# Optimization experiments

Hardware: AMD Instinct MI355X
Metric: run time of the kernel (lower is better)

Reference implementation:

```python
import jax, jax.numpy as jnp
import numpy as np

DN = ('NCHW', 'OIHW', 'NCHW')


def conv2d(x, w, b):
    y = jax.lax.conv_general_dilated(x, w, (1, 1), 'SAME', dimension_numbers=DN)
    return y + b[None, :, None, None]


def dyn_filter(x, Wa, ba, Wb, bb, Wc, bc):
    # KPN-style head: predict 81 per-pixel 9x9 filter taps, softmax-normalized.
    h = jax.nn.relu(conv2d(x, Wa, ba))
    h = jax.nn.relu(conv2d(h, Wb, bb))
    f = conv2d(h, Wc, bc)            # (N, 81, H, W)
    return jax.nn.softmax(f, axis=1)


def apply_dynamic_conv(x, f):
    # Equivalent to pad(4) + unfold(9x9) + mul + sum, without materializing
    # the (N,81,H,W)*... patch tensor: accumulate 81 shifted slices.
    N, C, H, W = x.shape  # C == 1
    xp = jnp.pad(x, ((0, 0), (0, 0), (4, 4), (4, 4)))
    out = jnp.zeros((N, 1, H, W), x.dtype)
    for dy in range(9):
        for dx in range(9):
            k = dy * 9 + dx  # matches unfold(2).unfold(3).permute(0,1,4,5,2,3) tap order
            out = out + xp[:, :, dy:dy + H, dx:dx + W] * f[:, k:k + 1]
    return out


def nearest_resize(x, oh, ow):
    _, _, ih, iw = x.shape
    ri = jnp.arange(oh) * ih // oh   # matches torch F.interpolate mode='nearest'
    rj = jnp.arange(ow) * iw // ow
    return x[:, :, ri][:, :, :, rj]


def setup_inputs() -> dict:
    key = jax.random.key(0)
    ks = jax.random.split(key, 8)
    s = 0.05
    return {
        'x': jax.random.normal(ks[0], (2, 1, 512, 512), jnp.float32),
        'g': jax.random.normal(ks[1], (2, 1, 512, 512), jnp.float32),
        'fWa': jax.random.normal(ks[2], (5, 64, 1, 3, 3), jnp.float32) * s,
        'fba': jnp.zeros((5, 64), jnp.float32),
        'fWb': jax.random.normal(ks[3], (5, 64, 64, 3, 3), jnp.float32) * s,
        'fbb': jnp.zeros((5, 64), jnp.float32),
        'fWc': jax.random.normal(ks[4], (5, 81, 64, 3, 3), jnp.float32) * s,
        'fbc': jnp.zeros((5, 81), jnp.float32),
        'W2a': jax.random.normal(ks[5], (64, 5, 3, 3), jnp.float32) * s,
        'b2a': jnp.zeros((64,), jnp.float32),
        'W2b': jax.random.normal(ks[6], (1, 64, 3, 3), jnp.float32) * s,
        'b2b': jnp.zeros((1,), jnp.float32),
    }


def reference(x, g, fWa, fba, fWb, fbb, fWc, fbc, W2a, b2a, W2b, b2b):
    N, C, h, w = x.shape
    scales = [
        x,
        nearest_resize(x, h // 2, w // 2),
        nearest_resize(x, h // 4, w // 4),
        nearest_resize(x, h // 8, w // 8),
        g,
    ]
    outs = []
    for i, s in enumerate(scales):
        f = dyn_filter(s, fWa[i], fba[i], fWb[i], fbb[i], fWc[i], fbc[i])
        y = apply_dynamic_conv(s, f)
        if y.shape[2] != h or y.shape[3] != w:
            y = nearest_resize(y, h, w)
        outs.append(y)
    cat = jnp.concatenate(outs, axis=1)  # (N, 5, h, w)
    hid = jax.nn.relu(conv2d(cat, W2a, b2a))
    return conv2d(hid, W2b, b2b)
```

## Files before the change

### kernel.cpp

```cpp
#include <hip/hip_runtime.h>
#include <math.h>

typedef _Float16 half8 __attribute__((ext_vector_type(8)));
typedef _Float16 half4v __attribute__((ext_vector_type(4)));
typedef float f32x4 __attribute__((ext_vector_type(4)));

#define LOG2E 1.44269504f

typedef __attribute__((address_space(1))) const unsigned int gas_u32;
typedef __attribute__((address_space(3))) unsigned int las_u32;

__device__ __forceinline__ void gll16(const void* gsrc, void* ldst) {
  __builtin_amdgcn_global_load_lds((gas_u32*)gsrc, (las_u32*)ldst, 16, 0, 0);
}
__device__ __forceinline__ void gll4(const void* gsrc, void* ldst) {
  __builtin_amdgcn_global_load_lds((gas_u32*)gsrc, (las_u32*)ldst, 4, 0, 0);
}

__device__ __forceinline__ void pack_generic(int rem, int NT, int COUT, float scale,
                                             const float* __restrict__ src,
                                             _Float16* __restrict__ dst) {
  int j = rem & 7, lane = (rem >> 3) & 63, rest = rem >> 9;
  int t = rest % NT, s = rest / NT;
  int oc = t * 16 + (lane & 15);
  int tap = s >> 1;
  int ic = (s & 1) * 32 + ((lane >> 4) & 3) * 8 + j;
  float v = (oc < COUT) ? src[((size_t)oc * 64 + ic) * 9 + tap] * scale : 0.f;
  dst[rem] = (_Float16)v;
}

__global__ void prep_all_kernel(const float* __restrict__ fWa, const float* __restrict__ fWb,
                                const float* __restrict__ fWc, const float* __restrict__ W2a,
                                const float* __restrict__ W2b, const float* __restrict__ x,
                                _Float16* __restrict__ Bp1, _Float16* __restrict__ BpA,
                                _Float16* __restrict__ BpB, _Float16* __restrict__ Bpb,
                                _Float16* __restrict__ Bpc,
                                _Float16* __restrict__ s1, _Float16* __restrict__ s2,
                                _Float16* __restrict__ s3) {
  int idx = blockIdx.x * blockDim.x + threadIdx.x;
  if (idx < 184320) {
    int sc = idx / 36864, rem = idx - sc * 36864;
    pack_generic(rem, 4, 64, 1.f, fWb + sc * 36864, Bpb + sc * 36864);
  } else if (idx < 460800) {
    int i2 = idx - 184320;
    int sc = i2 / 55296, rem = i2 - sc * 55296;
    pack_generic(rem, 6, 81, LOG2E, fWc + sc * 46656, Bpc + sc * 55296);
  } else if (idx < 471040) {
    int i2 = idx - 460800;
    int sc = i2 >> 11, rem = i2 & 2047;
    int j = rem & 7, lane = (rem >> 3) & 63, nt = rem >> 9;
    int oc = nt * 16 + (lane & 15);
    int k = ((lane >> 4) & 3) * 8 + j;
    float v = (k < 9) ? fWa[sc * 576 + oc * 9 + k] : 0.f;
    Bp1[sc * 2048 + rem] = (_Float16)v;
  } else if (idx < 475136) {
    int rem = idx - 471040;
    int j = rem & 7, lane = (rem >> 3) & 63;
    int nt = (rem >> 9) & 3, s = rem >> 11;
    int oc = nt * 16 + (lane & 15);
    int k = s * 32 + ((lane >> 4) & 3) * 8 + j;
    float v = 0.f;
    if (k < 45) { int ic = k / 9, tap = k - ic * 9; v = W2a[(oc * 5 + ic) * 9 + tap]; }
    BpA[rem] = (_Float16)v;
  } else if (idx < 484352) {
    pack_generic(idx - 475136, 1, 1, 1.f, W2b, BpB);
  } else if (idx < 615424) {
    int i2 = idx - 484352;
    int n = i2 >> 16, p = i2 & 65535, rr = p >> 8, cc = p & 255;
    s1[i2] = (_Float16)x[(size_t)n * 262144 + (size_t)(rr * 2) * 512 + cc * 2];
  } else if (idx < 648192) {
    int i2 = idx - 615424;
    int n = i2 >> 14, p = i2 & 16383, rr = p >> 7, cc = p & 127;
    s2[i2] = (_Float16)x[(size_t)n * 262144 + (size_t)(rr * 4) * 512 + cc * 4];
  } else if (idx < 656384) {
    int i2 = idx - 648192;
    int n = i2 >> 12, p = i2 & 4095, rr = p >> 6, cc = p & 63;
    s3[i2] = (_Float16)x[(size_t)n * 262144 + (size_t)(rr * 8) * 512 + cc * 8];
  }
}

__device__ __forceinline__ int xcd_swizzle(int bid) {
  return (bid & 7) * 596 + (bid >> 3);
}

__device__ __forceinline__ void map_block(int bid, int& sc, int& n, int& bx, int& by,
                                          int& Hs, int& RS, int& h2off) {
  if (bid < 2048) { sc = 0; Hs = 512; RS = 1; h2off = 0;
    int t = bid; n = t >> 10; t &= 1023; by = t >> 5; bx = t & 31; }
  else if (bid < 4096) { sc = 4; Hs = 512; RS = 1; h2off = 33554432;
    int t = bid - 2048; n = t >> 10; t &= 1023; by = t >> 5; bx = t & 31; }
  else if (bid < 4608) { sc = 1; Hs = 256; RS = 2; h2off = 67108864;
    int t = bid - 4096; n = t >> 8; t &= 255; by = t >> 4; bx = t & 15; }
  else if (bid < 4736) { sc = 2; Hs = 128; RS = 4; h2off = 75497472;
    int t = bid - 4608; n = t >> 6; t &= 63; by = t >> 3; bx = t & 7; }
  else { sc = 3; Hs = 64; RS = 8; h2off = 77594624;
    int t = bid - 4736; n = t >> 4; t &= 15; by = t >> 2; bx = t & 3; }
}

__device__ __forceinline__ const void* pick_src(int sc, const float* x, const float* g,
                                                const _Float16* s1, const _Float16* s2,
                                                const _Float16* s3, int& sStr, bool& f16s) {
  if (sc == 0) { sStr = 262144; f16s = false; return x; }
  if (sc == 1) { sStr = 65536; f16s = true; return s1; }
  if (sc == 2) { sStr = 16384; f16s = true; return s2; }
  if (sc == 3) { sStr = 4096; f16s = true; return s3; }
  sStr = 262144; f16s = false; return g;
}

__device__ __forceinline__ float src_load(const void* p, bool f16s, size_t off) {
  return f16s ? (float)((const _Float16*)p)[off] : ((const float*)p)[off];
}

template <int NT>
__device__ __forceinline__ void stageB_tap(const half8* __restrict__ Bp,
                                           _Float16* __restrict__ Bsd,
                                           int t, int buf, int tid) {
  const int lane = tid & 63, wv = tid >> 6;
  const char* s = (const char*)(Bp + (size_t)t * NT * 128) + wv * NT * 256 + lane * 4;
  char* d = (char*)Bsd + (size_t)buf * NT * 2048 + wv * NT * 256;
#pragma unroll
  for (int i = 0; i < NT; ++i) gll4(s + i * 256, d + i * 256);
}

template <int NT>
__device__ __forceinline__ void stageB01(const half8* __restrict__ Bp,
                                         _Float16* __restrict__ Bsd, int tid) {
  stageB_tap<NT>(Bp, Bsd, 0, 0, tid);
  stageB_tap<NT>(Bp, Bsd, 1, 1, tid);
}

template <int MT, int NT, bool SWAP>
__device__ __forceinline__ void tap_loop_counted(const _Float16* __restrict__ slab,
                                                 const half8* __restrict__ Bp,
                                                 _Float16* __restrict__ Bsd,
                                                 f32x4 (&acc)[MT][NT], int tid) {
  const int lane = tid & 63;
  const int wv = tid >> 6;
  const int quad = lane >> 4;
  const int ln15 = lane & 15;
  auto tap_body = [&](int t, int buf) {
    const int dy = t / 3, dx = t - dy * 3;
    const int C = dx + ln15;
    const int cx = C & 7;
    const _Float16* bb = Bsd + (size_t)buf * NT * 1024;
#pragma unroll
    for (int h = 0; h < 2; ++h) {
      half8 bf[NT];
#pragma unroll
      for (int nt = 0; nt < NT; ++nt)
        bf[nt] = *(const half8*)(bb + h * NT * 512 + (nt * 64 + lane) * 8);
      half8 af[MT];
#pragma unroll
      for (int mt = 0; mt < MT; ++mt) {
        const int px = (wv * MT + mt + dy) * 18 + C;
        af[mt] = *(const half8*)(slab + (size_t)px * 64 + ((h * 4 + quad) ^ cx) * 8);
      }
      __builtin_amdgcn_s_setprio(1);
#pragma unroll
      for (int mt = 0; mt < MT; ++mt)
#pragma unroll
        for (int nt = 0; nt < NT; ++nt)
          acc[mt][nt] = SWAP
            ? __builtin_amdgcn_mfma_f32_16x16x32_f16(bf[nt], af[mt], acc[mt][nt], 0, 0, 0)
            : __builtin_amdgcn_mfma_f32_16x16x32_f16(af[mt], bf[nt], acc[mt][nt], 0, 0, 0);
      __builtin_amdgcn_s_setprio(0);
    }
  };
#pragma unroll 1
  for (int t = 0; t < 8; ++t) {
    if (t >= 1) stageB_tap<NT>(Bp, Bsd, t + 1, (t + 1) & 1, tid);
    asm volatile("s_waitcnt vmcnt(%0)" :: "n"(NT) : "memory");
    __builtin_amdgcn_s_barrier();
    asm volatile("" ::: "memory");
    tap_body(t, t & 1);
    asm volatile("s_waitcnt lgkmcnt(0)" ::: "memory");
    __builtin_amdgcn_s_barrier();
    asm volatile("" ::: "memory");
  }
  asm volatile("s_waitcnt vmcnt(0)" ::: "memory");
  __builtin_amdgcn_s_barrier();
  asm volatile("" ::: "memory");
  tap_body(8, 0);
}

template <int MT, int NT, int COUT, int COUTP, bool RELU, typename OutT>
__device__ __forceinline__ void mfma_body(const _Float16* slab, const half8* __restrict__ Bp,
                                          _Float16* __restrict__ Bsd,
                                          const float* __restrict__ bias,
                                          OutT* __restrict__ out,
                                          int H, int W, int gr0, int gc0, int tid) {
  f32x4 acc[MT][NT];
  const f32x4 zz = {0.f, 0.f, 0.f, 0.f};
#pragma unroll
  for (int mt = 0; mt < MT; ++mt)
#pragma unroll
    for (int nt = 0; nt < NT; ++nt) acc[mt][nt] = zz;
  tap_loop_counted<MT, NT, false>(slab, Bp, Bsd, acc, tid);
  const int lane = tid & 63;
  const int wv = tid >> 6;
  const int quad = lane >> 4;
  const int ln15 = lane & 15;
  float bvv[NT];
#pragma unroll
  for (int nt = 0; nt < NT; ++nt) {
    const int oc = nt * 16 + ln15;
    bvv[nt] = (oc < COUT) ? bias[oc] : 0.f;
  }
#pragma unroll
  for (int mt = 0; mt < MT; ++mt) {
    const int gr = gr0 + wv * MT + mt;
#pragma unroll
    for (int reg = 0; reg < 4; ++reg) {
      const int gc = gc0 + quad * 4 + reg;
#pragma unroll
      for (int nt = 0; nt < NT; ++nt) {
        const int oc = nt * 16 + ln15;
        float v = acc[mt][nt][reg] + bvv[nt];
        if (RELU) v = fmaxf(v, 0.f);
        if (oc < COUTP) out[((size_t)gr * W + gc) * COUTP + oc] = (OutT)v;
      }
    }
  }
}

__global__ __launch_bounds__(512, 4)
void conv12_ms_kernel(const float* __restrict__ x, const float* __restrict__ g,
                      const _Float16* __restrict__ s1, const _Float16* __restrict__ s2,
                      const _Float16* __restrict__ s3,
                      const half8* __restrict__ Bp1b, const float* __restrict__ fba,
                      const half8* __restrict__ Bpbb, const float* __restrict__ fbb,
                      _Float16* __restrict__ h2) {
  __shared__ float xs[20 * 20];
  __shared__ __align__(16) _Float16 slab[18 * 18 * 64];
  __shared__ __align__(16) _Float16 BsS[2 * 4096];
  int sc, n, bx, by, Hs, RS, h2off;
  map_block(xcd_swizzle(blockIdx.x), sc, n, bx, by, Hs, RS, h2off);
  int sStr; bool f16s;
  const void* src = pick_src(sc, x, g, s1, s2, s3, sStr, f16s);
  _Float16* out = h2 + h2off + (size_t)n * Hs * Hs * 64;
  const half8* Bp1 = Bp1b + sc * 256;
  const half8* Bp = Bpbb + sc * 4608;
  const float* ba = fba + sc * 64;
  const float* bb = fbb + sc * 64;
  const int H = Hs, W = Hs;
  const int tid = threadIdx.x;
  const int gr0 = by * 16, gc0 = bx * 16;
  stageB01<4>(Bp, BsS, tid);
  for (int i = tid; i < 400; i += 512) {
    int R = i / 20, C = i % 20;
    int gr = gr0 - 2 + R, gc = gc0 - 2 + C;
    xs[i] = (gr >= 0 && gr < H && gc >= 0 && gc < W)
                ? src_load(src, f16s, (size_t)n * sStr + (size_t)gr * W + gc) : 0.f;
  }
  __syncthreads();
  const int lane = tid & 63;
  const int wv = tid >> 6;
  const int quad = lane >> 4;
  const int ln15 = lane & 15;
  half8 bf1[4];
  float b1v[4][4];
#pragma unroll
  for (int nt = 0; nt < 4; ++nt) {
    bf1[nt] = Bp1[nt * 64 + lane];
#pragma unroll
    for (int reg = 0; reg < 4; ++reg) b1v[nt][reg] = ba[nt * 16 + quad * 4 + reg];
  }
  int off1[8];
  bool v1[8];
#pragma unroll
  for (int j = 0; j < 8; ++j) {
    int k = quad * 8 + j;
    v1[j] = (k < 9);
    off1[j] = v1[j] ? ((k / 3) * 20 + (k % 3)) : 0;
  }
  const f32x4 zz = {0.f, 0.f, 0.f, 0.f};
#pragma unroll 1
  for (int mt = wv; mt < 21; mt += 8) {
    int p = mt * 16 + ln15;
    int pcl = (p < 323) ? p : 323;
    int Rg = pcl / 18, Cg = pcl - Rg * 18;
    int base = Rg * 20 + Cg;
    half8 af;
#pragma unroll
    for (int j = 0; j < 8; ++j)
      af[j] = v1[j] ? (_Float16)xs[base + off1[j]] : (_Float16)0.f;
    f32x4 a1[4] = {zz, zz, zz, zz};
#pragma unroll
    for (int nt = 0; nt < 4; ++nt)
      a1[nt] = __builtin_amdgcn_mfma_f32_16x16x32_f16(bf1[nt], af, a1[nt], 0, 0, 0);
    if (p < 324) {
      int R2 = p / 18, C2 = p - R2 * 18;
      int gr = gr0 - 1 + R2, gc = gc0 - 1 + C2;
      bool inb = (gr >= 0 && gr < H && gc >= 0 && gc < W);
      _Float16* sb = slab + p * 64 + (quad & 1) * 4;
      const int csw = C2 & 7;
#pragma unroll
      for (int nt = 0; nt < 4; ++nt) {
        half4v w;
#pragma unroll
        for (int reg = 0; reg < 4; ++reg) {
          float v = inb ? fmaxf(a1[nt][reg] + b1v[nt][reg], 0.f) : 0.f;
          w[reg] = (_Float16)v;
        }
        const int chunk = nt * 2 + (quad >> 1);
        *(half4v*)(sb + ((chunk ^ csw) * 8)) = w;
      }
    }
  }
  __syncthreads();
  mfma_body<2, 4, 64, 64, true, _Float16>(slab, Bp, BsS, bb, out, H, W, gr0, gc0, tid);
}

__global__ __launch_bounds__(512, 2)
void conv3sd_ms_kernel(const _Float16* __restrict__ h2, const half8* __restrict__ Bpcb,
                       const float* __restrict__ fbc,
                       const float* __restrict__ x, const float* __restrict__ g,
                       const _Float16* __restrict__ s1, const _Float16* __restrict__ s2,
                       const _Float16* __restrict__ s3, float* __restrict__ cat) {
  __shared__ __align__(16) _Float16 slab[384 * 64];
  __shared__ __align__(16) _Float16 Bsd[2 * 6144];
  __shared__ float xs[24 * 24];
  int sc, n, bx, by, Hs, RS, h2off;
  map_block(xcd_swizzle(blockIdx.x), sc, n, bx, by, Hs, RS, h2off);
  int sStr; bool f16s;
  const void* src = pick_src(sc, x, g, s1, s2, s3, sStr, f16s);
  const _Float16* in = h2 + h2off + (size_t)n * Hs * Hs * 64;
  const half8* Bp = Bpcb + sc * 6912;
  const float* bias = fbc + sc * 81;
  float* catp = cat + (size_t)(sc * 2 + n) * 262144;
  const int H = Hs, W = Hs;
  const int tid = threadIdx.x;
  const int gr0 = by * 16, gc0 = bx * 16;
  const int lane = tid & 63;
  const int wv = tid >> 6;
  const int quad = lane >> 4;
  const int ln15 = lane & 15;

  for (int i = tid; i < 576; i += 512) {
    int R = i / 24, C = i % 24;
    int gr = gr0 - 4 + R, gc = gc0 - 4 + C;
    xs[i] = (gr >= 0 && gr < H && gc >= 0 && gc < W)
                ? src_load(src, f16s, (size_t)n * sStr + (size_t)gr * W + gc) : 0.f;
  }

  const bool interior = (gr0 > 0) && (gc0 > 0) && (gr0 + 17 <= H) && (gc0 + 17 <= W);
  if (interior) {
    const int pxb0 = wv * 48;
#pragma unroll
    for (int k = 0; k < 6; ++k) {
      const int pxb = pxb0 + k * 8;
      int px = pxb + (lane >> 3);
      int pcl = (px < 324) ? px : 323;
      int R = pcl / 18, C = pcl - R * 18;
      int l = (lane & 7) ^ (C & 7);
      gll16((const char*)(in + ((size_t)(gr0 - 1 + R) * W + (gc0 - 1 + C)) * 64 + l * 8),
            (char*)slab + (size_t)pxb * 128);
    }
  } else {
    for (int i = tid; i < 2592; i += 512) {
      int px = i >> 3, pslot = i & 7;
      int R = px / 18, C = px - R * 18;
      int gr = gr0 - 1 + R, gc = gc0 - 1 + C;
      int l = pslot ^ (C & 7);
      half8 v = {0, 0, 0, 0, 0, 0, 0, 0};
      if (gr >= 0 && gr < H && gc >= 0 && gc < W)
        v = *(const half8*)(in + ((size_t)gr * W + gc) * 64 + l * 8);
      *(half8*)(slab + (size_t)px * 64 + pslot * 8) = v;
    }
  }

  stageB01<6>(Bp, Bsd, tid);
  asm volatile("s_waitcnt lgkmcnt(0)" ::: "memory");

  f32x4 acc[2][6];
  const f32x4 zz = {0.f, 0.f, 0.f, 0.f};
#pragma unroll
  for (int mt = 0; mt < 2; ++mt)
#pragma unroll
    for (int nt = 0; nt < 6; ++nt) acc[mt][nt] = zz;
  tap_loop_counted<2, 6, true>(slab, Bp, Bsd, acc, tid);

  float bvv[6][4];
  int dyx[6][4];
  bool vv[6][4];
#pragma unroll
  for (int nt = 0; nt < 6; ++nt)
#pragma unroll
    for (int reg = 0; reg < 4; ++reg) {
      int ch = nt * 16 + quad * 4 + reg;
      bool ok = (ch < 81);
      vv[nt][reg] = ok;
      bvv[nt][reg] = ok ? bias[ch] * LOG2E : 0.f;
      int dy = ch / 9, dx = ch - dy * 9;
      dyx[nt][reg] = ok ? dy * 24 + dx : 0;
    }
  const int lrs = (RS == 2) ? 1 : ((RS == 4) ? 2 : 3);
#pragma unroll
  for (int mt = 0; mt < 2; ++mt) {
    const float* xb = xs + (wv * 2 + mt) * 24 + ln15;
    float sum = 0.f, y = 0.f;
#pragma unroll
    for (int nt = 0; nt < 6; ++nt)
#pragma unroll
      for (int reg = 0; reg < 4; ++reg) {
        if (vv[nt][reg]) {
          float e = exp2f(acc[mt][nt][reg] + bvv[nt][reg]);
          sum += e;
          y = fmaf(e, xb[dyx[nt][reg]], y);
        }
      }
    sum += __shfl_xor(sum, 16, 64);
    sum += __shfl_xor(sum, 32, 64);
    y += __shfl_xor(y, 16, 64);
    y += __shfl_xor(y, 32, 64);
    const float o = y / sum;
    const int gr = gr0 + wv * 2 + mt, gc = gc0 + ln15;
    if (RS == 1) {
      if (quad == 0) catp[(size_t)gr * 512 + gc] = o;
    } else {
      for (int t = quad; t < RS * RS; t += 4) {
        int a = t >> lrs, b = t & (RS - 1);
        catp[((size_t)(gr * RS + a)) * 512 + (gc * RS + b)] = o;
      }
    }
  }
}

__global__ __launch_bounds__(512, 4)
void tail_fused_kernel(const float* __restrict__ cat,
                       const half8* __restrict__ BpA, const float* __restrict__ b2a,
                       const half8* __restrict__ BpB, const float* __restrict__ b2b,
                       float* __restrict__ out) {
  __shared__ float cs[20 * 20 * 5];
  __shared__ __align__(16) _Float16 hid[18 * 18 * 64];
  __shared__ __align__(16) _Float16 BsS[2 * 1024];
  const int n = blockIdx.z;
  float* op = out + (size_t)n * (512 * 512);
  const int tid = threadIdx.x;
  const int gr0 = blockIdx.y * 16, gc0 = blockIdx.x * 16;
  stageB01<1>(BpB, BsS, tid);
  for (int i = tid; i < 2000; i += 512) {
    int ic = i / 400, px = i - ic * 400;
    int R = px / 20, C = px - R * 20;
    int gr = gr0 - 2 + R, gc = gc0 - 2 + C;
    cs[px * 5 + ic] = (gr >= 0 && gr < 512 && gc >= 0 && gc < 512)
                ? cat[(size_t)(ic * 2 + n) * 262144 + (size_t)gr * 512 + gc] : 0.f;
  }
  __syncthreads();
  const int lane = tid & 63;
  const int wv = tid >> 6;
  const int quad = lane >> 4;
  const int ln15 = lane & 15;
  int goff[2][8];
  bool gok[2][8];
#pragma unroll
  for (int s = 0; s < 2; ++s)
#pragma unroll
    for (int j = 0; j < 8; ++j) {
      int k = s * 32 + quad * 8 + j;
      bool ok = (k < 45);
      int ic = k / 9;
      int tap = k - ic * 9;
      int dy = tap / 3, dx = tap - dy * 3;
      goff[s][j] = ok ? ((dy * 20 + dx) * 5 + ic) : 0;
      gok[s][j] = ok;
    }
  half8 bfA[2][4];
  float bAv[4][4];
#pragma unroll
  for (int s = 0; s < 2; ++s)
#pragma unroll
    for (int nt = 0; nt < 4; ++nt) bfA[s][nt] = BpA[(s * 4 + nt) * 64 + lane];
#pragma unroll
  for (int nt = 0; nt < 4; ++nt)
#pragma unroll
    for (int reg = 0; reg < 4; ++reg) bAv[nt][reg] = b2a[nt * 16 + quad * 4 + reg];
  const f32x4 zz = {0.f, 0.f, 0.f, 0.f};
#pragma unroll 1
  for (int mt = wv; mt < 21; mt += 8) {
    int p = mt * 16 + ln15;
    int pcl = (p < 323) ? p : 323;
    int base = (pcl / 18) * 100 + (pcl % 18) * 5;
    f32x4 acc1[4] = {zz, zz, zz, zz};
#pragma unroll
    for (int s = 0; s < 2; ++s) {
      half8 af;
#pragma unroll
      for (int j = 0; j < 8; ++j) {
        float a = gok[s][j] ? cs[base + goff[s][j]] : 0.f;
        af[j] = (_Float16)a;
      }
#pragma unroll
      for (int nt = 0; nt < 4; ++nt)
        acc1[nt] = __builtin_amdgcn_mfma_f32_16x16x32_f16(bfA[s][nt], af, acc1[nt], 0, 0, 0);
    }
    if (p < 324) {
      int R2 = p / 18, C2 = p - R2 * 18;
      int gr = gr0 - 1 + R2, gc = gc0 - 1 + C2;
      bool inb = (gr >= 0 && gr < 512 && gc >= 0 && gc < 512);
      _Float16* sb = hid + p * 64 + (quad & 1) * 4;
      const int csw = C2 & 7;
#pragma unroll
      for (int nt = 0; nt < 4; ++nt) {
        half4v w;
#pragma unroll
        for (int reg = 0; reg < 4; ++reg) {
          float v = inb ? fmaxf(acc1[nt][reg] + bAv[nt][reg], 0.f) : 0.f;
          w[reg] = (_Float16)v;
        }
        const int chunk = nt * 2 + (quad >> 1);
        *(half4v*)(sb + ((chunk ^ csw) * 8)) = w;
      }
    }
  }
  __syncthreads();
  mfma_body<2, 1, 1, 1, false, float>(hid, BpB, BsS, b2b, op, 512, 512, gr0, gc0, tid);
}

extern "C" void kernel_launch(void* const* d_in, const int* in_sizes, int n_in,
                              void* d_out, int out_size, void* d_ws, size_t ws_size,
                              hipStream_t stream) {
  (void)in_sizes; (void)n_in; (void)out_size; (void)ws_size;
  const float* x   = (const float*)d_in[0];
  const float* g   = (const float*)d_in[1];
  const float* fWa = (const float*)d_in[2];
  const float* fba = (const float*)d_in[3];
  const float* fWb = (const float*)d_in[4];
  const float* fbb = (const float*)d_in[5];
  const float* fWc = (const float*)d_in[6];
  const float* fbc = (const float*)d_in[7];
  const float* W2a = (const float*)d_in[8];
  const float* b2a = (const float*)d_in[9];
  const float* W2b = (const float*)d_in[10];
  const float* b2b = (const float*)d_in[11];
  float* out = (float*)d_out;
  float* ws = (float*)d_ws;

  float* Bp1F = ws;
  float* BpAF = Bp1F + 5120;
  float* BpBF = BpAF + 2048;
  float* BpbF = BpBF + 4608;
  float* BpcF = BpbF + 92160;
  float* s1F  = BpcF + 138240;
  float* s2F  = s1F + 65536;
  float* s3F  = s2F + 16384;
  float* cat  = s3F + 4096;
  float* h2F  = cat + 2621440;
  _Float16* s1 = (_Float16*)s1F;
  _Float16* s2 = (_Float16*)s2F;
  _Float16* s3 = (_Float16*)s3F;
  _Float16* h2 = (_Float16*)h2F;
  const half8* Bp1 = (const half8*)Bp1F;
  const half8* BpA = (const half8*)BpAF;
  const half8* BpB = (const half8*)BpBF;
  const half8* Bpb = (const half8*)BpbF;
  const half8* Bpc = (const half8*)BpcF;

  prep_all_kernel<<<2564, 256, 0, stream>>>(fWa, fWb, fWc, W2a, W2b, x,
                                            (_Float16*)Bp1F, (_Float16*)BpAF,
                                            (_Float16*)BpBF, (_Float16*)BpbF,
                                            (_Float16*)BpcF, s1, s2, s3);
  conv12_ms_kernel<<<4768, 512, 0, stream>>>(x, g, s1, s2, s3, Bp1, fba, Bpb, fbb, h2);
  conv3sd_ms_kernel<<<4768, 512, 0, stream>>>(h2, Bpc, fbc, x, g, s1, s2, s3, cat);
  tail_fused_kernel<<<dim3(32, 32, 2), 512, 0, stream>>>(cat, BpA, b2a, BpB, b2b, out);
}
```

Baseline: 377.1 us.

## Fuse conv1/conv2 with conv3 and dynamic filter, removing h2 global round trip

Merges the conv12 and conv3sd kernels into one per-tile kernel. Conv1 is computed on a 20x20 halo, conv2 on an 18x18 halo, and conv3 plus the softmax dynamic filter then run directly from LDS. This removes the fp16 h2 intermediate write and read through global memory, plus one kernel launch. In exchange it recomputes halo pixels, raises LDS use to about 92KB, which limits occupancy to one block per CU (launch bounds 512,1). Conv2 weights now come from global/L2 per step instead of staged LDS.

```diff
diff --git a/kernel.cpp b/kernel.cpp
--- a/kernel.cpp
+++ b/kernel.cpp
@@ -10,9 +10,6 @@
 typedef __attribute__((address_space(1))) const unsigned int gas_u32;
 typedef __attribute__((address_space(3))) unsigned int las_u32;
 
-__device__ __forceinline__ void gll16(const void* gsrc, void* ldst) {
-  __builtin_amdgcn_global_load_lds((gas_u32*)gsrc, (las_u32*)ldst, 16, 0, 0);
-}
 __device__ __forceinline__ void gll4(const void* gsrc, void* ldst) {
   __builtin_amdgcn_global_load_lds((gas_u32*)gsrc, (las_u32*)ldst, 4, 0, 0);
 }
@@ -84,16 +81,16 @@
 }
 
 __device__ __forceinline__ void map_block(int bid, int& sc, int& n, int& bx, int& by,
-                                          int& Hs, int& RS, int& h2off) {
-  if (bid < 2048) { sc = 0; Hs = 512; RS = 1; h2off = 0;
+                                          int& Hs, int& RS) {
+  if (bid < 2048) { sc = 0; Hs = 512; RS = 1;
     int t = bid; n = t >> 10; t &= 1023; by = t >> 5; bx = t & 31; }
-  else if (bid < 4096) { sc = 4; Hs = 512; RS = 1; h2off = 33554432;
+  else if (bid < 4096) { sc = 4; Hs = 512; RS = 1;
     int t = bid - 2048; n = t >> 10; t &= 1023; by = t >> 5; bx = t & 31; }
-  else if (bid < 4608) { sc = 1; Hs = 256; RS = 2; h2off = 67108864;
+  else if (bid < 4608) { sc = 1; Hs = 256; RS = 2;
     int t = bid - 4096; n = t >> 8; t &= 255; by = t >> 4; bx = t & 15; }
-  else if (bid < 4736) { sc = 2; Hs = 128; RS = 4; h2off = 75497472;
+  else if (bid < 4736) { sc = 2; Hs = 128; RS = 4;
     int t = bid - 4608; n = t >> 6; t &= 63; by = t >> 3; bx = t & 7; }
-  else { sc = 3; Hs = 64; RS = 8; h2off = 77594624;
+  else { sc = 3; Hs = 64; RS = 8;
     int t = bid - 4736; n = t >> 4; t &= 15; by = t >> 2; bx = t & 3; }
 }
 
@@ -223,109 +220,28 @@
   }
 }
 
-__global__ __launch_bounds__(512, 4)
-void conv12_ms_kernel(const float* __restrict__ x, const float* __restrict__ g,
-                      const _Float16* __restrict__ s1, const _Float16* __restrict__ s2,
-                      const _Float16* __restrict__ s3,
-                      const half8* __restrict__ Bp1b, const float* __restrict__ fba,
-                      const half8* __restrict__ Bpbb, const float* __restrict__ fbb,
-                      _Float16* __restrict__ h2) {
-  __shared__ float xs[20 * 20];
-  __shared__ __align__(16) _Float16 slab[18 * 18 * 64];
-  __shared__ __align__(16) _Float16 BsS[2 * 4096];
-  int sc, n, bx, by, Hs, RS, h2off;
-  map_block(xcd_swizzle(blockIdx.x), sc, n, bx, by, Hs, RS, h2off);
+__global__ __launch_bounds__(512, 1)
+void fused_ms_kernel(const float* __restrict__ x, const float* __restrict__ g,
+                     const _Float16* __restrict__ s1, const _Float16* __restrict__ s2,
+                     const _Float16* __restrict__ s3,
+                     const half8* __restrict__ Bp1b, const float* __restrict__ fba,
+                     const half8* __restrict__ Bpbb, const float* __restrict__ fbb,
+                     const half8* __restrict__ Bpcb, const float* __restrict__ fbc,
+                     float* __restrict__ cat) {
+  __shared__ float xs[24 * 24];
+  __shared__ __align__(16) _Float16 slabA[400 * 64];
+  __shared__ __align__(16) _Float16 slabB[324 * 64];
+  _Float16* Bsd = slabA;
+
+  int sc, n, bx, by, Hs, RS;
+  map_block(xcd_swizzle(blockIdx.x), sc, n, bx, by, Hs, RS);
   int sStr; bool f16s;
   const void* src = pick_src(sc, x, g, s1, s2, s3, sStr, f16s);
-  _Float16* out = h2 + h2off + (size_t)n * Hs * Hs * 64;
   const half8* Bp1 = Bp1b + sc * 256;
-  const half8* Bp = Bpbb + sc * 4608;
+  const half8* Bpb = Bpbb + sc * 4608;
+  const half8* Bpc = Bpcb + sc * 6912;
   const float* ba = fba + sc * 64;
   const float* bb = fbb + sc * 64;
-  const int H = Hs, W = Hs;
-  const int tid = threadIdx.x;
-  const int gr0 = by * 16, gc0 = bx * 16;
-  stageB01<4>(Bp, BsS, tid);
-  for (int i = tid; i < 400; i += 512) {
-    int R = i / 20, C = i % 20;
-    int gr = gr0 - 2 + R, gc = gc0 - 2 + C;
-    xs[i] = (gr >= 0 && gr < H && gc >= 0 && gc < W)
-                ? src_load(src, f16s, (size_t)n * sStr + (size_t)gr * W + gc) : 0.f;
-  }
-  __syncthreads();
-  const int lane = tid & 63;
-  const int wv = tid >> 6;
-  const int quad = lane >> 4;
-  const int ln15 = lane & 15;
-  half8 bf1[4];
-  float b1v[4][4];
-#pragma unroll
-  for (int nt = 0; nt < 4; ++nt) {
-    bf1[nt] = Bp1[nt * 64 + lane];
-#pragma unroll
-    for (int reg = 0; reg < 4; ++reg) b1v[nt][reg] = ba[nt * 16 + quad * 4 + reg];
-  }
-  int off1[8];
-  bool v1[8];
-#pragma unroll
-  for (int j = 0; j < 8; ++j) {
-    int k = quad * 8 + j;
-    v1[j] = (k < 9);
-    off1[j] = v1[j] ? ((k / 3) * 20 + (k % 3)) : 0;
-  }
-  const f32x4 zz = {0.f, 0.f, 0.f, 0.f};
-#pragma unroll 1
-  for (int mt = wv; mt < 21; mt += 8) {
-    int p = mt * 16 + ln15;
-    int pcl = (p < 323) ? p : 323;
-    int Rg = pcl / 18, Cg = pcl - Rg * 18;
-    int base = Rg * 20 + Cg;
-    half8 af;
-#pragma unroll
-    for (int j = 0; j < 8; ++j)
-      af[j] = v1[j] ? (_Float16)xs[base + off1[j]] : (_Float16)0.f;
-    f32x4 a1[4] = {zz, zz, zz, zz};
-#pragma unroll
-    for (int nt = 0; nt < 4; ++nt)
-      a1[nt] = __builtin_amdgcn_mfma_f32_16x16x32_f16(bf1[nt], af, a1[nt], 0, 0, 0);
-    if (p < 324) {
-      int R2 = p / 18, C2 = p - R2 * 18;
-      int gr = gr0 - 1 + R2, gc = gc0 - 1 + C2;
-      bool inb = (gr >= 0 && gr < H && gc >= 0 && gc < W);
-      _Float16* sb = slab + p * 64 + (quad & 1) * 4;
-      const int csw = C2 & 7;
-#pragma unroll
-      for (int nt = 0; nt < 4; ++nt) {
-        half4v w;
-#pragma unroll
-        for (int reg = 0; reg < 4; ++reg) {
-          float v = inb ? fmaxf(a1[nt][reg] + b1v[nt][reg], 0.f) : 0.f;
-          w[reg] = (_Float16)v;
-        }
-        const int chunk = nt * 2 + (quad >> 1);
-        *(half4v*)(sb + ((chunk ^ csw) * 8)) = w;
-      }
-    }
-  }
-  __syncthreads();
-  mfma_body<2, 4, 64, 64, true, _Float16>(slab, Bp, BsS, bb, out, H, W, gr0, gc0, tid);
-}
-
-__global__ __launch_bounds__(512, 2)
-void conv3sd_ms_kernel(const _Float16* __restrict__ h2, const half8* __restrict__ Bpcb,
-                       const float* __restrict__ fbc,
-                       const float* __restrict__ x, const float* __restrict__ g,
-                       const _Float16* __restrict__ s1, const _Float16* __restrict__ s2,
-                       const _Float16* __restrict__ s3, float* __restrict__ cat) {
-  __shared__ __align__(16) _Float16 slab[384 * 64];
-  __shared__ __align__(16) _Float16 Bsd[2 * 6144];
-  __shared__ float xs[24 * 24];
-  int sc, n, bx, by, Hs, RS, h2off;
-  map_block(xcd_swizzle(blockIdx.x), sc, n, bx, by, Hs, RS, h2off);
-  int sStr; bool f16s;
-  const void* src = pick_src(sc, x, g, s1, s2, s3, sStr, f16s);
-  const _Float16* in = h2 + h2off + (size_t)n * Hs * Hs * 64;
-  const half8* Bp = Bpcb + sc * 6912;
   const float* bias = fbc + sc * 81;
   float* catp = cat + (size_t)(sc * 2 + n) * 262144;
   const int H = Hs, W = Hs;
@@ -342,43 +258,125 @@
     xs[i] = (gr >= 0 && gr < H && gc >= 0 && gc < W)
                 ? src_load(src, f16s, (size_t)n * sStr + (size_t)gr * W + gc) : 0.f;
   }
-
-  const bool interior = (gr0 > 0) && (gc0 > 0) && (gr0 + 17 <= H) && (gc0 + 17 <= W);
-  if (interior) {
-    const int pxb0 = wv * 48;
-#pragma unroll
-    for (int k = 0; k < 6; ++k) {
-      const int pxb = pxb0 + k * 8;
-      int px = pxb + (lane >> 3);
-      int pcl = (px < 324) ? px : 323;
-      int R = pcl / 18, C = pcl - R * 18;
-      int l = (lane & 7) ^ (C & 7);
-      gll16((const char*)(in + ((size_t)(gr0 - 1 + R) * W + (gc0 - 1 + C)) * 64 + l * 8),
-            (char*)slab + (size_t)pxb * 128);
-    }
-  } else {
-    for (int i = tid; i < 2592; i += 512) {
-      int px = i >> 3, pslot = i & 7;
-      int R = px / 18, C = px - R * 18;
-      int gr = gr0 - 1 + R, gc = gc0 - 1 + C;
-      int l = pslot ^ (C & 7);
-      half8 v = {0, 0, 0, 0, 0, 0, 0, 0};
-      if (gr >= 0 && gr < H && gc >= 0 && gc < W)
-        v = *(const half8*)(in + ((size_t)gr * W + gc) * 64 + l * 8);
-      *(half8*)(slab + (size_t)px * 64 + pslot * 8) = v;
-    }
-  }
-
-  stageB01<6>(Bp, Bsd, tid);
-  asm volatile("s_waitcnt lgkmcnt(0)" ::: "memory");
-
+  __syncthreads();
+
+  {
+    half8 bf1[4];
+    float b1v[4][4];
+#pragma unroll
+    for (int nt = 0; nt < 4; ++nt) {
+      bf1[nt] = Bp1[nt * 64 + lane];
+#pragma unroll
+      for (int reg = 0; reg < 4; ++reg) b1v[nt][reg] = ba[nt * 16 + quad * 4 + reg];
+    }
+    int off1[8];
+    bool v1[8];
+#pragma unroll
+    for (int j = 0; j < 8; ++j) {
+      int k = quad * 8 + j;
+      v1[j] = (k < 9);
+      off1[j] = v1[j] ? ((k / 3) * 24 + (k % 3)) : 0;
+    }
+    const f32x4 zz = {0.f, 0.f, 0.f, 0.f};
+#pragma unroll 1
+    for (int mt = wv; mt < 25; mt += 8) {
+      int p = mt * 16 + ln15;
+      int RA = p / 20, CA = p - RA * 20;
+      int base = (RA + 1) * 24 + (CA + 1);
+      half8 af;
+#pragma unroll
+      for (int j = 0; j < 8; ++j)
+        af[j] = v1[j] ? (_Float16)xs[base + off1[j]] : (_Float16)0.f;
+      f32x4 a1[4] = {zz, zz, zz, zz};
+#pragma unroll
+      for (int nt = 0; nt < 4; ++nt)
+        a1[nt] = __builtin_amdgcn_mfma_f32_16x16x32_f16(bf1[nt], af, a1[nt], 0, 0, 0);
+      int gr = gr0 - 2 + RA, gc = gc0 - 2 + CA;
+      bool inb = (gr >= 0 && gr < H && gc >= 0 && gc < W);
+      _Float16* sb = slabA + (size_t)p * 64 + (quad & 1) * 4;
+      const int csw = CA & 7;
+#pragma unroll
+      for (int nt = 0; nt < 4; ++nt) {
+        half4v w;
+#pragma unroll
+        for (int reg = 0; reg < 4; ++reg) {
+          float v = inb ? fmaxf(a1[nt][reg] + b1v[nt][reg], 0.f) : 0.f;
+          w[reg] = (_Float16)v;
+        }
+        const int chunk = nt * 2 + (quad >> 1);
+        *(half4v*)(sb + ((chunk ^ csw) * 8)) = w;
+      }
+    }
+  }
+  __syncthreads();
+
+  {
+    float b2v[4][4];
+#pragma unroll
+    for (int nt = 0; nt < 4; ++nt)
+#pragma unroll
+      for (int reg = 0; reg < 4; ++reg) b2v[nt][reg] = bb[nt * 16 + quad * 4 + reg];
+    const f32x4 zz = {0.f, 0.f, 0.f, 0.f};
+#pragma unroll 1
+    for (int mt = wv; mt < 21; mt += 8) {
+      int p = mt * 16 + ln15;
+      int pcl = (p < 323) ? p : 323;
+      int R3 = pcl / 18, C3 = pcl - R3 * 18;
+      f32x4 a2[4] = {zz, zz, zz, zz};
+      auto step = [&](int s, half8 (&bf)[4]) {
+        const int tap = s >> 1, h = s & 1;
+        const int dy = tap / 3, dx = tap - dy * 3;
+        const int CA2 = C3 + dx;
+        const int pA = (R3 + dy) * 20 + CA2;
+        const int qsw = ((h * 4 + quad) ^ (CA2 & 7));
+        half8 af = *(const half8*)(slabA + (size_t)pA * 64 + qsw * 8);
+#pragma unroll
+        for (int nt = 0; nt < 4; ++nt)
+          a2[nt] = __builtin_amdgcn_mfma_f32_16x16x32_f16(bf[nt], af, a2[nt], 0, 0, 0);
+      };
+      half8 bA[4], bB[4];
+#pragma unroll
+      for (int nt = 0; nt < 4; ++nt) bA[nt] = Bpb[nt * 64 + lane];
+#pragma unroll 1
+      for (int i = 0; i < 9; ++i) {
+        const int sA = 2 * i + 1;
+        const int sB = (sA + 1 < 18) ? sA + 1 : 17;
+#pragma unroll
+        for (int nt = 0; nt < 4; ++nt) bB[nt] = Bpb[(sA * 4 + nt) * 64 + lane];
+        step(2 * i, bA);
+#pragma unroll
+        for (int nt = 0; nt < 4; ++nt) bA[nt] = Bpb[(sB * 4 + nt) * 64 + lane];
+        step(sA, bB);
+      }
+      if (p < 324) {
+        int gr = gr0 - 1 + R3, gc = gc0 - 1 + C3;
+        bool inb = (gr >= 0 && gr < H && gc >= 0 && gc < W);
+        _Float16* sb = slabB + (size_t)p * 64 + (quad & 1) * 4;
+        const int csw = C3 & 7;
+#pragma unroll
+        for (int nt = 0; nt < 4; ++nt) {
+          half4v w;
+#pragma unroll
+          for (int reg = 0; reg < 4; ++reg) {
+            float v = inb ? fmaxf(a2[nt][reg] + b2v[nt][reg], 0.f) : 0.f;
+            w[reg] = (_Float16)v;
+          }
+          const int chunk = nt * 2 + (quad >> 1);
+          *(half4v*)(sb + ((chunk ^ csw) * 8)) = w;
+        }
+      }
+    }
+  }
+  __syncthreads();
+
+  stageB01<6>(Bpc, Bsd, tid);
   f32x4 acc[2][6];
   const f32x4 zz = {0.f, 0.f, 0.f, 0.f};
 #pragma unroll
   for (int mt = 0; mt < 2; ++mt)
 #pragma unroll
     for (int nt = 0; nt < 6; ++nt) acc[mt][nt] = zz;
-  tap_loop_counted<2, 6, true>(slab, Bp, Bsd, acc, tid);
+  tap_loop_counted<2, 6, true>(slabB, Bpc, Bsd, acc, tid);
 
   float bvv[6][4];
   int dyx[6][4];
@@ -545,11 +543,9 @@
   float* s2F  = s1F + 65536;
   float* s3F  = s2F + 16384;
   float* cat  = s3F + 4096;
-  float* h2F  = cat + 2621440;
   _Float16* s1 = (_Float16*)s1F;
   _Float16* s2 = (_Float16*)s2F;
   _Float16* s3 = (_Float16*)s3F;
-  _Float16* h2 = (_Float16*)h2F;
   const half8* Bp1 = (const half8*)Bp1F;
   const half8* BpA = (const half8*)BpAF;
   const half8* BpB = (const half8*)BpBF;
@@ -560,7 +556,7 @@
                                             (_Float16*)Bp1F, (_Float16*)BpAF,
                                             (_Float16*)BpBF, (_Float16*)BpbF,
                                             (_Float16*)BpcF, s1, s2, s3);
-  conv12_ms_kernel<<<4768, 512, 0, stream>>>(x, g, s1, s2, s3, Bp1, fba, Bpb, fbb, h2);
-  conv3sd_ms_kernel<<<4768, 512, 0, stream>>>(h2, Bpc, fbc, x, g, s1, s2, s3, cat);
+  fused_ms_kernel<<<4768, 512, 0, stream>>>(x, g, s1, s2, s3, Bp1, fba, Bpb, fbb,
+                                            Bpc, fbc, cat);
   tail_fused_kernel<<<dim3(32, 32, 2), 512, 0, stream>>>(cat, BpA, b2a, BpB, b2b, out);
 }
```

New measurement: 598.5 us. 1.59x slower.
